# Kernel tuning notes

Measured on AMD Instinct MI355X. Metric: run time of the kernel, lower is better.

Reference implementation:

```python
import jax, jax.numpy as jnp
import numpy as np

B, S, D, H = 2, 2048, 1024, 16
DK = D // H

def setup_inputs() -> dict:
    key = jax.random.key(0)
    ks = jax.random.split(key, 9)
    scale = 1.0 / np.sqrt(D)
    return {
        "x": jax.random.normal(ks[0], (B, S, D), dtype=jnp.float32),
        "Wq": jax.random.uniform(ks[1], (D, D), jnp.float32, -scale, scale),
        "bq": jax.random.uniform(ks[2], (D,), jnp.float32, -scale, scale),
        "Wk": jax.random.uniform(ks[3], (D, D), jnp.float32, -scale, scale),
        "bk": jax.random.uniform(ks[4], (D,), jnp.float32, -scale, scale),
        "Wv": jax.random.uniform(ks[5], (D, D), jnp.float32, -scale, scale),
        "bv": jax.random.uniform(ks[6], (D,), jnp.float32, -scale, scale),
        "Wo": jax.random.uniform(ks[7], (D, D), jnp.float32, -scale, scale),
        "bo": jax.random.uniform(ks[8], (D,), jnp.float32, -scale, scale),
    }

def reference(x, Wq, bq, Wk, bk, Wv, bv, Wo, bo):
    # QKV projections (torch Linear: x @ W.T + b)
    q = x @ Wq.T + bq
    k = x @ Wk.T + bk
    v = x @ Wv.T + bv
    # [B, H, S, DK]
    q = q.reshape(B, S, H, DK).transpose(0, 2, 1, 3)
    k = k.reshape(B, S, H, DK).transpose(0, 2, 1, 3)
    v = v.reshape(B, S, H, DK).transpose(0, 2, 1, 3)
    scores = jnp.einsum('bhqd,bhkd->bhqk', q, k) / jnp.sqrt(jnp.float32(DK))
    p = jax.nn.softmax(scores, axis=-1)  # dropout is identity in eval mode
    o = jnp.einsum('bhqk,bhkd->bhqd', p, v)
    o = o.transpose(0, 2, 1, 3).reshape(B, S, D)
    return o @ Wo.T + bo
```

## Files before the change

kernel.cpp:

```cpp
#include <hip/hip_runtime.h>
#include <hip/hip_bf16.h>


typedef __attribute__((ext_vector_type(8))) short short8;
typedef __attribute__((ext_vector_type(4))) float f32x4;
typedef __attribute__((ext_vector_type(4))) unsigned int u32x4;
typedef __attribute__((ext_vector_type(8))) unsigned short u16x8;

__device__ __forceinline__ unsigned short f2bf(float f) {
    unsigned int u = __builtin_bit_cast(unsigned int, f);
    u += 0x7FFFu + ((u >> 16) & 1u);
    return (unsigned short)(u >> 16);
}

__device__ __forceinline__ unsigned short bfc(float f) {
    return __builtin_bit_cast(unsigned short, __float2bfloat16(f));
}

__device__ __forceinline__ float exp2_fast(float x) {
    return __builtin_amdgcn_exp2f(x);
}

__device__ __forceinline__ void gload16(const void* gsrc, void* ldst) {
    __builtin_amdgcn_global_load_lds(
        (const __attribute__((address_space(1))) unsigned int*)gsrc,
        (__attribute__((address_space(3))) unsigned int*)ldst, 16, 0, 0);
}

__global__ void cast_all(const float* __restrict__ x,
                         const float* __restrict__ wq, const float* __restrict__ wk,
                         const float* __restrict__ wv, const float* __restrict__ wo,
                         unsigned short* __restrict__ xb,
                         unsigned short* __restrict__ wqb, unsigned short* __restrict__ wkb,
                         unsigned short* __restrict__ wvb, unsigned short* __restrict__ wob)
{
    const int z = blockIdx.y;
    const float* src; unsigned short* dst; int n4;
    if (z == 0)      { src = x;  dst = xb;  n4 = 4096 * 1024 / 4; }
    else if (z == 1) { src = wq; dst = wqb; n4 = 1024 * 1024 / 4; }
    else if (z == 2) { src = wk; dst = wkb; n4 = 1024 * 1024 / 4; }
    else if (z == 3) { src = wv; dst = wvb; n4 = 1024 * 1024 / 4; }
    else             { src = wo; dst = wob; n4 = 1024 * 1024 / 4; }
    int i = blockIdx.x * blockDim.x + threadIdx.x;
    if (i < n4) {
        float4 v = reinterpret_cast<const float4*>(src)[i];
        ushort4 o;
        o.x = f2bf(v.x); o.y = f2bf(v.y); o.z = f2bf(v.z); o.w = f2bf(v.w);
        reinterpret_cast<ushort4*>(dst)[i] = o;
    }
}

__global__ __launch_bounds__(256, 2)
void qkv_gemm(const unsigned short* __restrict__ A,
              const unsigned short* __restrict__ Wq_,
              const unsigned short* __restrict__ Wk_,
              const unsigned short* __restrict__ Wv_,
              const float* __restrict__ bq_,
              const float* __restrict__ bk_,
              const float* __restrict__ bv_,
              unsigned short* __restrict__ Qb,
              unsigned short* __restrict__ Kb,
              unsigned short* __restrict__ Vtb)
{
    const int K = 1024;
    __shared__ __align__(16) unsigned short As[128][64];
    __shared__ __align__(16) unsigned short Bs[128][64];

    const int z = blockIdx.z;
    const unsigned short* Bw = (z == 0) ? Wq_ : (z == 1) ? Wk_ : Wv_;
    const float* bias = (z == 0) ? bq_ : (z == 1) ? bk_ : bv_;
    unsigned short* dst = (z == 0) ? Qb : (z == 1) ? Kb : Vtb;
    const float alpha = (z == 0) ? 0.125f * 1.44269504088896340736f : 1.0f;

    const int tid  = threadIdx.x;
    const int lane = tid & 63;
    const int wave = tid >> 6;
    const int wm = (wave >> 1) * 64;
    const int wn = (wave & 1) * 64;
    const int rowBase = blockIdx.y * 128;
    const int colBase = blockIdx.x * 128;
    const int l15 = lane & 15;
    const int lg  = lane >> 4;

    const int srow   = lane >> 3;
    const int schunk = lane & 7;
    const int gchunk = schunk ^ srow;

    f32x4 acc[4][4] = {};

    for (int kt = 0; kt < K; kt += 64) {
        __syncthreads();
#pragma unroll
        for (int it = 0; it < 4; ++it) {
            int r = wave * 8 + it * 32 + srow;
            gload16(A  + (size_t)(rowBase + r) * K + kt + gchunk * 8, &As[wave * 8 + it * 32][0]);
            gload16(Bw + (size_t)(colBase + r) * K + kt + gchunk * 8, &Bs[wave * 8 + it * 32][0]);
        }
        __syncthreads();
#pragma unroll
        for (int kk = 0; kk < 2; ++kk) {
            short8 af[4], bf[4];
#pragma unroll
            for (int fm = 0; fm < 4; ++fm) {
                int r  = wm + fm * 16 + l15;
                int kb = (kk * 4 + lg) ^ (r & 7);
                af[fm] = *reinterpret_cast<const short8*>(&As[r][kb * 8]);
            }
#pragma unroll
            for (int fn = 0; fn < 4; ++fn) {
                int r  = wn + fn * 16 + l15;
                int kb = (kk * 4 + lg) ^ (r & 7);
                bf[fn] = *reinterpret_cast<const short8*>(&Bs[r][kb * 8]);
            }
#pragma unroll
            for (int fm = 0; fm < 4; ++fm)
#pragma unroll
                for (int fn = 0; fn < 4; ++fn)
                    acc[fm][fn] = __builtin_amdgcn_mfma_f32_16x16x32_bf16(
                        af[fm], bf[fn], acc[fm][fn], 0, 0, 0);
        }
    }

#pragma unroll
    for (int fm = 0; fm < 4; ++fm)
#pragma unroll
        for (int fn = 0; fn < 4; ++fn)
#pragma unroll
            for (int r = 0; r < 4; ++r) {
                int grow = rowBase + wm + fm * 16 + lg * 4 + r;
                int gcol = colBase + wn + fn * 16 + l15;
                float v = (acc[fm][fn][r] + bias[gcol]) * alpha;
                int b = grow >> 11, s = grow & 2047;
                int h = gcol >> 6,  dk = gcol & 63;
                if (z < 2)
                    dst[(((size_t)b * 16 + h) * 2048 + s) * 64 + dk] = f2bf(v);
                else
                    dst[(((size_t)b * 16 + h) * 64 + dk) * 2048 + s] = f2bf(v);
            }
}

__global__ __launch_bounds__(256, 2)
void gemm_out(const unsigned short* __restrict__ A,
              const unsigned short* __restrict__ Bw,
              const float* __restrict__ bias,
              float* __restrict__ Cout, int M, int N, int K)
{
    __shared__ __align__(16) unsigned short As[128][64];
    __shared__ __align__(16) unsigned short Bs[64][64];

    const int tid  = threadIdx.x;
    const int lane = tid & 63;
    const int wave = tid >> 6;
    const int wm = (wave >> 1) * 64;
    const int wn = (wave & 1) * 32;
    const int rowBase = blockIdx.y * 128;
    const int colBase = blockIdx.x * 64;
    const int l15 = lane & 15;
    const int lg  = lane >> 4;

    const int srow   = lane >> 3;
    const int schunk = lane & 7;
    const int gchunk = schunk ^ srow;

    f32x4 acc[4][2] = {};

    for (int kt = 0; kt < K; kt += 64) {
        __syncthreads();
#pragma unroll
        for (int it = 0; it < 4; ++it) {
            int r = wave * 8 + it * 32 + srow;
            gload16(A + (size_t)(rowBase + r) * K + kt + gchunk * 8, &As[wave * 8 + it * 32][0]);
        }
#pragma unroll
        for (int it = 0; it < 2; ++it) {
            int rb = wave * 16 + it * 8;
            int r  = rb + srow;
            gload16(Bw + (size_t)(colBase + r) * K + kt + gchunk * 8, &Bs[rb][0]);
        }
        __syncthreads();
#pragma unroll
        for (int kk = 0; kk < 2; ++kk) {
            short8 af[4], bf[2];
#pragma unroll
            for (int fm = 0; fm < 4; ++fm) {
                int r  = wm + fm * 16 + l15;
                int kb = (kk * 4 + lg) ^ (r & 7);
                af[fm] = *reinterpret_cast<const short8*>(&As[r][kb * 8]);
            }
#pragma unroll
            for (int fn = 0; fn < 2; ++fn) {
                int r  = wn + fn * 16 + l15;
                int kb = (kk * 4 + lg) ^ (r & 7);
                bf[fn] = *reinterpret_cast<const short8*>(&Bs[r][kb * 8]);
            }
#pragma unroll
            for (int fm = 0; fm < 4; ++fm)
#pragma unroll
                for (int fn = 0; fn < 2; ++fn)
                    acc[fm][fn] = __builtin_amdgcn_mfma_f32_16x16x32_bf16(
                        af[fm], bf[fn], acc[fm][fn], 0, 0, 0);
        }
    }

#pragma unroll
    for (int fm = 0; fm < 4; ++fm)
#pragma unroll
        for (int fn = 0; fn < 2; ++fn)
#pragma unroll
            for (int r = 0; r < 4; ++r) {
                int grow = rowBase + wm + fm * 16 + lg * 4 + r;
                int gcol = colBase + wn + fn * 16 + l15;
                Cout[(size_t)grow * N + gcol] = acc[fm][fn][r] + bias[gcol];
            }
}

__global__ __launch_bounds__(256, 2)
void attn_kernel(const unsigned short* __restrict__ Q,
                 const unsigned short* __restrict__ Kt,
                 const unsigned short* __restrict__ Vt,
                 unsigned short* __restrict__ O)
{
    __shared__ __align__(16) unsigned short Ks[2][128][64];
    __shared__ __align__(16) unsigned short Vs[2][64][128];

    const int lid = blockIdx.x + 16 * blockIdx.y;
    const int bh  = 4 * (lid & 7) + ((lid >> 3) & 3);
    const int qt  = lid >> 5;
    const int tid  = threadIdx.x;
    const int lane = tid & 63;
    const int w    = tid >> 6;
    const int l15 = lane & 15;
    const int lg  = lane >> 4;

    const unsigned short* Qbh = Q  + (size_t)bh * 2048 * 64;
    const unsigned short* Kbh = Kt + (size_t)bh * 2048 * 64;
    const unsigned short* Vbh = Vt + (size_t)bh * 64 * 2048;

    short8 qf[2][2];
#pragma unroll
    for (int fq = 0; fq < 2; ++fq)
#pragma unroll
        for (int kk = 0; kk < 2; ++kk) {
            int row = qt * 128 + w * 32 + fq * 16 + l15;
            qf[fq][kk] = *reinterpret_cast<const short8*>(
                Qbh + (size_t)row * 64 + kk * 32 + lg * 8);
        }

    short8 ones;
#pragma unroll
    for (int j = 0; j < 8; ++j) ones[j] = (short)0x3F80;

    f32x4 accO[2][4] = {};
    f32x4 accSum[2] = {};

    const int sr  = tid >> 3, skb = tid & 7;
    const int vr  = tid >> 4, vkb = tid & 15;

    u16x8 kst[4], vst[4];
#pragma unroll
    for (int it = 0; it < 4; ++it)
        kst[it] = *reinterpret_cast<const u16x8*>(Kbh + (size_t)(sr + it * 32) * 64 + skb * 8);
#pragma unroll
    for (int it = 0; it < 4; ++it)
        vst[it] = *reinterpret_cast<const u16x8*>(Vbh + (size_t)(vr + it * 16) * 2048 + vkb * 8);

    int cur = 0;
    for (int t = 0; t < 16; ++t) {
#pragma unroll
        for (int it = 0; it < 4; ++it) {
            int r = sr + it * 32;
            *reinterpret_cast<u16x8*>(&Ks[cur][r][(skb ^ (r & 7)) * 8]) = kst[it];
        }
#pragma unroll
        for (int it = 0; it < 4; ++it) {
            int r = vr + it * 16;
            *reinterpret_cast<u16x8*>(&Vs[cur][r][(vkb ^ (r & 15)) * 8]) = vst[it];
        }
        __syncthreads();

        if (t < 15) {
#pragma unroll
            for (int it = 0; it < 4; ++it)
                kst[it] = *reinterpret_cast<const u16x8*>(
                    Kbh + (size_t)((t + 1) * 128 + sr + it * 32) * 64 + skb * 8);
#pragma unroll
            for (int it = 0; it < 4; ++it)
                vst[it] = *reinterpret_cast<const u16x8*>(
                    Vbh + (size_t)(vr + it * 16) * 2048 + (t + 1) * 128 + vkb * 8);
        }

        f32x4 accS[8][2] = {};
#pragma unroll
        for (int kk = 0; kk < 2; ++kk) {
            short8 kf[8];
#pragma unroll
            for (int fk = 0; fk < 8; ++fk) {
                int r  = fk * 16 + l15;
                int kb = (kk * 4 + lg) ^ (r & 7);
                kf[fk] = *reinterpret_cast<const short8*>(&Ks[cur][r][kb * 8]);
            }
#pragma unroll
            for (int fk = 0; fk < 8; ++fk)
#pragma unroll
                for (int fq = 0; fq < 2; ++fq)
                    accS[fk][fq] = __builtin_amdgcn_mfma_f32_16x16x32_bf16(
                        kf[fk], qf[fq][kk], accS[fk][fq], 0, 0, 0);
        }

#pragma unroll
        for (int hh = 0; hh < 2; ++hh) {
            unsigned int plo[2][4], phi[2][4];
#pragma unroll
            for (int fq = 0; fq < 2; ++fq)
#pragma unroll
                for (int f2 = 0; f2 < 4; ++f2) {
                    int fk = hh * 4 + f2;
                    float p0 = exp2_fast(accS[fk][fq][0]);
                    float p1 = exp2_fast(accS[fk][fq][1]);
                    float p2 = exp2_fast(accS[fk][fq][2]);
                    float p3 = exp2_fast(accS[fk][fq][3]);
                    plo[fq][f2] = (unsigned int)bfc(p0) | ((unsigned int)bfc(p1) << 16);
                    phi[fq][f2] = (unsigned int)bfc(p2) | ((unsigned int)bfc(p3) << 16);
                }

#pragma unroll
            for (int k2 = 0; k2 < 2; ++k2) {
                short8 vf[4];
#pragma unroll
                for (int fd = 0; fd < 4; ++fd) {
                    int row = fd * 16 + l15;
                    int kb  = ((hh * 2 + k2) * 4 + lg) ^ (row & 15);
                    vf[fd] = *reinterpret_cast<const short8*>(&Vs[cur][row][kb * 8]);
                }
#pragma unroll
                for (int fq = 0; fq < 2; ++fq) {
                    unsigned int Alo = plo[fq][2 * k2], Blo = plo[fq][2 * k2 + 1];
                    auto r1 = __builtin_amdgcn_permlane32_swap(Alo, Blo, false, false);
                    auto r2 = __builtin_amdgcn_permlane16_swap(r1[0], r1[1], false, false);
                    unsigned int Ahi = phi[fq][2 * k2], Bhi = phi[fq][2 * k2 + 1];
                    auto r3 = __builtin_amdgcn_permlane32_swap(Ahi, Bhi, false, false);
                    auto r4 = __builtin_amdgcn_permlane16_swap(r3[0], r3[1], false, false);
                    u32x4 fw;
                    fw[0] = r2[0];
                    fw[1] = r4[0];
                    fw[2] = r2[1];
                    fw[3] = r4[1];
                    short8 pf = __builtin_bit_cast(short8, fw);
#pragma unroll
                    for (int fd = 0; fd < 4; ++fd)
                        accO[fq][fd] = __builtin_amdgcn_mfma_f32_16x16x32_bf16(
                            pf, vf[fd], accO[fq][fd], 0, 0, 0);
                    accSum[fq] = __builtin_amdgcn_mfma_f32_16x16x32_bf16(
                        pf, ones, accSum[fq], 0, 0, 0);
                }
            }
        }

        cur ^= 1;
    }

    const int b = bh >> 4, h = bh & 15;
#pragma unroll
    for (int fq = 0; fq < 2; ++fq)
#pragma unroll
        for (int r = 0; r < 4; ++r) {
            float linv = 1.0f / accSum[fq][r];
            int s = qt * 128 + w * 32 + fq * 16 + lg * 4 + r;
#pragma unroll
            for (int fd = 0; fd < 4; ++fd) {
                int dk = fd * 16 + l15;
                O[((size_t)b * 2048 + s) * 1024 + h * 64 + dk] = f2bf(accO[fq][fd][r] * linv);
            }
        }
}

extern "C" void kernel_launch(void* const* d_in, const int* in_sizes, int n_in,
                              void* d_out, int out_size, void* d_ws, size_t ws_size,
                              hipStream_t stream)
{
    const float* x  = (const float*)d_in[0];
    const float* Wq = (const float*)d_in[1];
    const float* bq = (const float*)d_in[2];
    const float* Wk = (const float*)d_in[3];
    const float* bk = (const float*)d_in[4];
    const float* Wv = (const float*)d_in[5];
    const float* bv = (const float*)d_in[6];
    const float* Wo = (const float*)d_in[7];
    const float* bo = (const float*)d_in[8];
    float* out = (float*)d_out;

    char* ws = (char*)d_ws;
    unsigned short* xb  = (unsigned short*)(ws);
    unsigned short* wqb = (unsigned short*)(ws + ((size_t)8  << 20));
    unsigned short* wkb = (unsigned short*)(ws + ((size_t)10 << 20));
    unsigned short* wvb = (unsigned short*)(ws + ((size_t)12 << 20));
    unsigned short* wob = (unsigned short*)(ws + ((size_t)14 << 20));
    unsigned short* Qb  = (unsigned short*)(ws + ((size_t)16 << 20));
    unsigned short* Kb  = (unsigned short*)(ws + ((size_t)24 << 20));
    unsigned short* Vtb = (unsigned short*)(ws + ((size_t)32 << 20));
    unsigned short* Ob  = (unsigned short*)(ws + ((size_t)40 << 20));

    cast_all<<<dim3(4096, 5), 256, 0, stream>>>(x, Wq, Wk, Wv, Wo,
                                                xb, wqb, wkb, wvb, wob);

    qkv_gemm<<<dim3(8, 32, 3), 256, 0, stream>>>(xb, wqb, wkb, wvb, bq, bk, bv,
                                                 Qb, Kb, Vtb);

    attn_kernel<<<dim3(16, 32), 256, 0, stream>>>(Qb, Kb, Vtb, Ob);

    gemm_out<<<dim3(16, 32), 256, 0, stream>>>(Ob, wob, bo, out, 4096, 1024, 1024);
}
```

Measured before the change: 111.9 us.

## Remap GEMM blocks per XCD, add MFMA priority and hoist V loads in attention

Both GEMM kernels now remap the linear block id so that consecutive row tiles land on the same XCD, which should raise L2 reuse of shared A and weight tiles. The attention kernel wraps its MFMA sections in s_setprio so waves issuing matrix work get scheduling priority. It also loads all V fragments for a half-tile before the exp/pack stage, giving the LDS reads time to complete behind the ALU work. Holding the hoisted fragments raises register pressure, and the remap assumes the fixed grid shapes.

```diff
diff --git a/kernel.cpp b/kernel.cpp
--- a/kernel.cpp
+++ b/kernel.cpp
@@ -66,7 +66,14 @@
     __shared__ __align__(16) unsigned short As[128][64];
     __shared__ __align__(16) unsigned short Bs[128][64];
 
-    const int z = blockIdx.z;
+    const int lid = blockIdx.x + 8 * blockIdx.y + 256 * blockIdx.z;
+    const int xcd = lid & 7;
+    const int j   = lid >> 3;
+    const int z   = j >> 5;
+    const int rr  = j & 31;
+    const int by  = xcd * 4 + (rr >> 3);
+    const int bx  = rr & 7;
+
     const unsigned short* Bw = (z == 0) ? Wq_ : (z == 1) ? Wk_ : Wv_;
     const float* bias = (z == 0) ? bq_ : (z == 1) ? bk_ : bv_;
     unsigned short* dst = (z == 0) ? Qb : (z == 1) ? Kb : Vtb;
@@ -77,8 +84,8 @@
     const int wave = tid >> 6;
     const int wm = (wave >> 1) * 64;
     const int wn = (wave & 1) * 64;
-    const int rowBase = blockIdx.y * 128;
-    const int colBase = blockIdx.x * 128;
+    const int rowBase = by * 128;
+    const int colBase = bx * 128;
     const int l15 = lane & 15;
     const int lg  = lane >> 4;
 
@@ -148,13 +155,19 @@
     __shared__ __align__(16) unsigned short As[128][64];
     __shared__ __align__(16) unsigned short Bs[64][64];
 
+    const int lid = blockIdx.x + 16 * blockIdx.y;
+    const int xcd = lid & 7;
+    const int j   = lid >> 3;
+    const int by  = xcd * 4 + (j >> 4);
+    const int bx  = j & 15;
+
     const int tid  = threadIdx.x;
     const int lane = tid & 63;
     const int wave = tid >> 6;
     const int wm = (wave >> 1) * 64;
     const int wn = (wave & 1) * 32;
-    const int rowBase = blockIdx.y * 128;
-    const int colBase = blockIdx.x * 64;
+    const int rowBase = by * 128;
+    const int colBase = bx * 64;
     const int l15 = lane & 15;
     const int lg  = lane >> 4;
 
@@ -299,16 +312,28 @@
                 int kb = (kk * 4 + lg) ^ (r & 7);
                 kf[fk] = *reinterpret_cast<const short8*>(&Ks[cur][r][kb * 8]);
             }
+            __builtin_amdgcn_s_setprio(1);
 #pragma unroll
             for (int fk = 0; fk < 8; ++fk)
 #pragma unroll
                 for (int fq = 0; fq < 2; ++fq)
                     accS[fk][fq] = __builtin_amdgcn_mfma_f32_16x16x32_bf16(
                         kf[fk], qf[fq][kk], accS[fk][fq], 0, 0, 0);
+            __builtin_amdgcn_s_setprio(0);
         }
 
 #pragma unroll
         for (int hh = 0; hh < 2; ++hh) {
+            short8 vfh[2][4];
+#pragma unroll
+            for (int k2 = 0; k2 < 2; ++k2)
+#pragma unroll
+                for (int fd = 0; fd < 4; ++fd) {
+                    int row = fd * 16 + l15;
+                    int kb  = ((hh * 2 + k2) * 4 + lg) ^ (row & 15);
+                    vfh[k2][fd] = *reinterpret_cast<const short8*>(&Vs[cur][row][kb * 8]);
+                }
+
             unsigned int plo[2][4], phi[2][4];
 #pragma unroll
             for (int fq = 0; fq < 2; ++fq)
@@ -323,15 +348,9 @@
                     phi[fq][f2] = (unsigned int)bfc(p2) | ((unsigned int)bfc(p3) << 16);
                 }
 
+            __builtin_amdgcn_s_setprio(1);
 #pragma unroll
             for (int k2 = 0; k2 < 2; ++k2) {
-                short8 vf[4];
-#pragma unroll
-                for (int fd = 0; fd < 4; ++fd) {
-                    int row = fd * 16 + l15;
-                    int kb  = ((hh * 2 + k2) * 4 + lg) ^ (row & 15);
-                    vf[fd] = *reinterpret_cast<const short8*>(&Vs[cur][row][kb * 8]);
-                }
 #pragma unroll
                 for (int fq = 0; fq < 2; ++fq) {
                     unsigned int Alo = plo[fq][2 * k2], Blo = plo[fq][2 * k2 + 1];
@@ -349,11 +368,12 @@
 #pragma unroll
                     for (int fd = 0; fd < 4; ++fd)
                         accO[fq][fd] = __builtin_amdgcn_mfma_f32_16x16x32_bf16(
-                            pf, vf[fd], accO[fq][fd], 0, 0, 0);
+                            pf, vfh[k2][fd], accO[fq][fd], 0, 0, 0);
                     accSum[fq] = __builtin_amdgcn_mfma_f32_16x16x32_bf16(
                         pf, ones, accSum[fq], 0, 0, 0);
                 }
             }
+            __builtin_amdgcn_s_setprio(0);
         }
 
         cur ^= 1;
```

After: 113.4 us. Within noise of the previous version (+1.3%).
